# Kernel optimization log

Measured on AMD Instinct MI355X. Metric: run time of the kernel, lower is better.

Reference implementation:

```python
import jax, jax.numpy as jnp
import numpy as np

EMBED = 1024
HEADS = 16
HEAD_DIM = EMBED // HEADS
LN_EPS = 1e-5


def _layer_norm(x, g, b):
    m = jnp.mean(x, axis=-1, keepdims=True)
    v = jnp.mean((x - m) ** 2, axis=-1, keepdims=True)
    return (x - m) / jnp.sqrt(v + LN_EPS) * g + b


def _rope(x):
    # x: (b, H, n, D); standard rotary: freqs repeated (cat(freqs, freqs)), rotate_half
    D = x.shape[-1]
    n = x.shape[2]
    inv_freq = 1.0 / (10000.0 ** (jnp.arange(0, D, 2, dtype=jnp.float32) / D))
    freqs = jnp.arange(n, dtype=jnp.float32)[:, None] * inv_freq[None, :]  # (n, D/2)
    emb = jnp.concatenate([freqs, freqs], axis=-1)  # (n, D)
    cos, sin = jnp.cos(emb), jnp.sin(emb)
    rot = jnp.concatenate([-x[..., D // 2:], x[..., : D // 2]], axis=-1)
    return x * cos + rot * sin


def setup_inputs() -> dict:
    key = jax.random.key(0)
    ks = jax.random.split(key, 8)
    E = EMBED
    s_in = 1.0 / np.sqrt(E)
    return {
        "x": jax.random.normal(ks[0], (2, 2048, E), dtype=jnp.float32),
        "in_proj_w": jax.random.uniform(ks[1], (3 * E, E), jnp.float32, -s_in, s_in),
        "in_proj_b": jnp.zeros((3 * E,), jnp.float32),
        "out_proj_w": jax.random.uniform(ks[2], (E, E), jnp.float32, -s_in, s_in),
        "out_proj_b": jnp.zeros((E,), jnp.float32),
        "geglu_w": jax.random.uniform(ks[3], (2 * E, E), jnp.float32, -s_in, s_in),
        "geglu_b": jnp.zeros((2 * E,), jnp.float32),
        "ln1_g": jnp.ones((E,), jnp.float32),
        "ln1_b": jnp.zeros((E,), jnp.float32),
        "ln2_g": jnp.ones((E,), jnp.float32),
        "ln2_b": jnp.zeros((E,), jnp.float32),
    }


def reference(x, in_proj_w, in_proj_b, out_proj_w, out_proj_b,
              geglu_w, geglu_b, ln1_g, ln1_b, ln2_g, ln2_b):
    b, n, E = x.shape
    H, D = HEADS, HEAD_DIM

    # RoPE applied to raw x (q = k = v = x in the module)
    xh = x.reshape(b, n, H, D).transpose(0, 2, 1, 3)  # (b,H,n,D)
    qr = _rope(xh)
    kr = qr  # q and k are identical pre-projection
    q = qr.transpose(0, 2, 1, 3).reshape(b, n, E)
    k = kr.transpose(0, 2, 1, 3).reshape(b, n, E)
    v = x

    # MultiheadAttention (batch-first semantics): in-proj, per-head SDPA, out-proj
    w_q, w_k, w_v = jnp.split(in_proj_w, 3, axis=0)
    b_q, b_k, b_v = jnp.split(in_proj_b, 3, axis=0)
    qp = (q @ w_q.T + b_q).reshape(b, n, H, D).transpose(0, 2, 1, 3)
    kp = (k @ w_k.T + b_k).reshape(b, n, H, D).transpose(0, 2, 1, 3)
    vp = (v @ w_v.T + b_v).reshape(b, n, H, D).transpose(0, 2, 1, 3)
    scores = jnp.einsum("bhqd,bhkd->bhqk", qp, kp) / jnp.sqrt(jnp.float32(D))
    attn = jax.nn.softmax(scores, axis=-1)
    ctx = jnp.einsum("bhqk,bhkd->bhqd", attn, vp)
    ctx = ctx.transpose(0, 2, 1, 3).reshape(b, n, E)
    attn_out = ctx @ out_proj_w.T + out_proj_b

    # residual + LN1
    h = _layer_norm(x + attn_out, ln1_g, ln1_b)

    # GeGLU: Linear(E -> 2E), chunk, value * gelu(gate) (exact erf gelu like torch)
    proj = h @ geglu_w.T + geglu_b
    val, gate = jnp.split(proj, 2, axis=-1)
    fc_out = val * jax.nn.gelu(gate, approximate=False)

    # residual + LN2
    return _layer_norm(h + fc_out, ln2_g, ln2_b)
```

## Files before the change

kernel.cpp:

```cpp
#include <hip/hip_runtime.h>


typedef __bf16 bf16;
typedef bf16 bf16x8 __attribute__((ext_vector_type(8)));
typedef bf16 bf16x4 __attribute__((ext_vector_type(4)));
typedef float f32x4 __attribute__((ext_vector_type(4)));
typedef float f32x16 __attribute__((ext_vector_type(16)));

#define EMB 1024
#define SEQ 2048
#define NTOK 4096
#define NH 16
#define HD 64

__device__ __forceinline__ f32x4 mfma16(bf16x8 a, bf16x8 b, f32x4 c) {
  return __builtin_amdgcn_mfma_f32_16x16x32_bf16(a, b, c, 0, 0, 0);
}
__device__ __forceinline__ f32x16 mfma32(bf16x8 a, bf16x8 b, f32x16 c) {
  return __builtin_amdgcn_mfma_f32_32x32x16_bf16(a, b, c, 0, 0, 0);
}

__device__ __forceinline__ void gll16(const void* g, void* l) {
  __builtin_amdgcn_global_load_lds(
      (const __attribute__((address_space(1))) void*)g,
      (__attribute__((address_space(3))) void*)l, 16, 0, 0);
}

__device__ __forceinline__ unsigned pk2(float a, float b) {
  union { bf16 h[2]; unsigned u; } t;
  t.h[0] = (bf16)a; t.h[1] = (bf16)b;
  return t.u;
}


__global__ __launch_bounds__(256) void rope_cast(
    const float* __restrict__ x, bf16* __restrict__ xb, bf16* __restrict__ qr) {
  int idx = blockIdx.x * 256 + threadIdx.x;
  int row = idx >> 9;
  int i = idx & 511;
  int h = i >> 5, d2 = i & 31;
  int pos = row & (SEQ - 1);
  int c0 = h * HD + d2;
  size_t base = (size_t)row * EMB;
  float x0 = x[base + c0], x1 = x[base + c0 + 32];
  float invf = exp2f(-(float)d2 * 0.4152410118609203f);
  float ang = (float)pos * invf;
  float sn, cs;
  sincosf(ang, &sn, &cs);
  qr[base + c0] = (bf16)(x0 * cs - x1 * sn);
  qr[base + c0 + 32] = (bf16)(x1 * cs + x0 * sn);
  xb[base + c0] = (bf16)x0;
  xb[base + c0 + 32] = (bf16)x1;
}

__global__ __launch_bounds__(256) void cast_w(
    const float* __restrict__ w, bf16* __restrict__ o, int n) {
  int i = (blockIdx.x * 256 + threadIdx.x) * 4;
  if (i < n) {
    float4 f = *(const float4*)(w + i);
    o[i] = (bf16)f.x; o[i + 1] = (bf16)f.y;
    o[i + 2] = (bf16)f.z; o[i + 3] = (bf16)f.w;
  }
}

__global__ __launch_bounds__(256) void gemm_in(
    const bf16* __restrict__ Aq, const bf16* __restrict__ Ax,
    const bf16* __restrict__ W, const float* __restrict__ bias,
    bf16* __restrict__ qb, bf16* __restrict__ kv) {
  __shared__ bf16 As[128 * 32];
  __shared__ bf16 Bs[128 * 32];
  const int tid = threadIdx.x, lane = tid & 63, wave = tid >> 6;
  const int quad = lane >> 4, l16 = lane & 15;
  const int m0 = blockIdx.y * 128, n0 = blockIdx.x * 128;
  const bf16* A = (n0 < 2048) ? Aq : Ax;
  const int K = 1024;
  const int wm = (wave >> 1) * 64, wn = (wave & 1) * 64;
  const int srow = wave * 32 + (lane >> 2);
  const int scol = (lane & 3) * 8;
  f32x4 acc[4][4] = {};
  for (int k0 = 0; k0 < K; k0 += 32) {
    __syncthreads();
    gll16(A + (size_t)(m0 + srow) * K + k0 + scol, As + wave * 1024);
    gll16(A + (size_t)(m0 + srow + 16) * K + k0 + scol, As + wave * 1024 + 512);
    gll16(W + (size_t)(n0 + srow) * K + k0 + scol, Bs + wave * 1024);
    gll16(W + (size_t)(n0 + srow + 16) * K + k0 + scol, Bs + wave * 1024 + 512);
    __syncthreads();
    bf16x8 af[4], bw[4];
#pragma unroll
    for (int t = 0; t < 4; ++t) {
      af[t] = *(const bf16x8*)(As + (wm + t * 16 + l16) * 32 + quad * 8);
      bw[t] = *(const bf16x8*)(Bs + (wn + t * 16 + l16) * 32 + quad * 8);
    }
#pragma unroll
    for (int mt = 0; mt < 4; ++mt)
#pragma unroll
      for (int nt = 0; nt < 4; ++nt)
        acc[mt][nt] = mfma16(af[mt], bw[nt], acc[mt][nt]);
  }
  if (n0 < 1024) {
#pragma unroll
    for (int mt = 0; mt < 4; ++mt)
      for (int nt = 0; nt < 4; ++nt) {
        const int n = n0 + wn + nt * 16 + l16;
        const float bv = bias[n];
#pragma unroll
        for (int r = 0; r < 4; ++r) {
          const int m = m0 + wm + mt * 16 + quad * 4 + r;
          qb[(size_t)m * 1024 + n] = (bf16)((acc[mt][nt][r] + bv) * 0.125f);
        }
      }
  } else if (n0 < 2048) {
#pragma unroll
    for (int mt = 0; mt < 4; ++mt)
      for (int nt = 0; nt < 4; ++nt) {
        const int n = n0 + wn + nt * 16 + l16;
        const float bv = bias[n];
        const int kd = n - 1024, hh = kd >> 6, d = kd & 63;
        const int dc = d >> 3, dl = d & 7;
#pragma unroll
        for (int r = 0; r < 4; ++r) {
          const int m = m0 + wm + mt * 16 + quad * 4 + r;
          const int bb = m >> 11, s = m & 2047;
          const int t = s >> 7, kr = s & 127;
          const size_t base = ((size_t)((bb * 16 + hh) * 16 + t)) * 16384;
          kv[base + kr * 64 + ((dc ^ (kr & 7)) << 3) + dl] =
              (bf16)((acc[mt][nt][r] + bv) * 1.4426950408889634f);
        }
      }
  } else {
#pragma unroll
    for (int mt = 0; mt < 4; ++mt)
      for (int nt = 0; nt < 4; ++nt) {
        const int n = n0 + wn + nt * 16 + l16;
        const float bv = bias[n];
        const int vd = n - 2048, hh = vd >> 6, d = vd & 63;
        const int m = m0 + wm + mt * 16 + quad * 4;
        const int bb = m >> 11, s = m & 2047;
        const int t = s >> 7, kt = s & 127;
        const int g = kt >> 4, w = kt & 15;
        const int c = 2 * g + ((w >> 2) & 1);
        const int slot = (w & 8) ? 4 : 0;
        const size_t base = ((size_t)((bb * 16 + hh) * 16 + t)) * 16384 + 8192;
        bf16x4 pkv;
#pragma unroll
        for (int r = 0; r < 4; ++r) pkv[r] = (bf16)(acc[mt][nt][r] + bv);
        *(bf16x4*)(kv + base + d * 128 + ((c ^ (d & 7)) << 3) + slot) = pkv;
      }
  }
}

__global__ __launch_bounds__(256) void gemm_bt(
    const bf16* __restrict__ A, const bf16* __restrict__ W,
    const float* __restrict__ bias,
    float* __restrict__ outF, bf16* __restrict__ outB,
    int M, int N, int K) {
  __shared__ bf16 As[128 * 32];
  __shared__ bf16 Bs[128 * 32];
  const int tid = threadIdx.x, lane = tid & 63, wave = tid >> 6;
  const int quad = lane >> 4, l16 = lane & 15;
  const int m0 = blockIdx.y * 128, n0 = blockIdx.x * 128;
  const int wm = (wave >> 1) * 64, wn = (wave & 1) * 64;
  const int srow = wave * 32 + (lane >> 2);
  const int scol = (lane & 3) * 8;
  f32x4 acc[4][4] = {};
  for (int k0 = 0; k0 < K; k0 += 32) {
    __syncthreads();
    gll16(A + (size_t)(m0 + srow) * K + k0 + scol, As + wave * 1024);
    gll16(A + (size_t)(m0 + srow + 16) * K + k0 + scol, As + wave * 1024 + 512);
    gll16(W + (size_t)(n0 + srow) * K + k0 + scol, Bs + wave * 1024);
    gll16(W + (size_t)(n0 + srow + 16) * K + k0 + scol, Bs + wave * 1024 + 512);
    __syncthreads();
    bf16x8 af[4], bw[4];
#pragma unroll
    for (int t = 0; t < 4; ++t) {
      af[t] = *(const bf16x8*)(As + (wm + t * 16 + l16) * 32 + quad * 8);
      bw[t] = *(const bf16x8*)(Bs + (wn + t * 16 + l16) * 32 + quad * 8);
    }
#pragma unroll
    for (int mt = 0; mt < 4; ++mt)
#pragma unroll
      for (int nt = 0; nt < 4; ++nt)
        acc[mt][nt] = mfma16(af[mt], bw[nt], acc[mt][nt]);
  }
#pragma unroll
  for (int mt = 0; mt < 4; ++mt)
    for (int nt = 0; nt < 4; ++nt) {
      const int n = n0 + wn + nt * 16 + l16;
      const float bv = bias ? bias[n] : 0.0f;
#pragma unroll
      for (int r = 0; r < 4; ++r) {
        const int m = m0 + wm + mt * 16 + quad * 4 + r;
        const float v = acc[mt][nt][r] + bv;
        if (outF) outF[(size_t)m * N + n] = v;
        if (outB) outB[(size_t)m * N + n] = (bf16)v;
      }
    }
}

__global__ __launch_bounds__(256) void gemm_bt64(
    const bf16* __restrict__ A, const bf16* __restrict__ W,
    const float* __restrict__ bias, float* __restrict__ outF,
    int M, int N, int K) {
  __shared__ bf16 As[128 * 32];
  __shared__ bf16 Bs[64 * 32];
  const int tid = threadIdx.x, lane = tid & 63, wave = tid >> 6;
  const int quad = lane >> 4, l16 = lane & 15;
  const int m0 = blockIdx.y * 128, n0 = blockIdx.x * 64;
  const int wm = (wave >> 1) * 64, wn = (wave & 1) * 32;
  const int srow = wave * 32 + (lane >> 2);
  const int srowB = wave * 16 + (lane >> 2);
  const int scol = (lane & 3) * 8;
  f32x4 acc[4][2] = {};
  for (int k0 = 0; k0 < K; k0 += 32) {
    __syncthreads();
    gll16(A + (size_t)(m0 + srow) * K + k0 + scol, As + wave * 1024);
    gll16(A + (size_t)(m0 + srow + 16) * K + k0 + scol, As + wave * 1024 + 512);
    gll16(W + (size_t)(n0 + srowB) * K + k0 + scol, Bs + wave * 512);
    __syncthreads();
    bf16x8 af[4], bw[2];
#pragma unroll
    for (int t = 0; t < 4; ++t)
      af[t] = *(const bf16x8*)(As + (wm + t * 16 + l16) * 32 + quad * 8);
#pragma unroll
    for (int t = 0; t < 2; ++t)
      bw[t] = *(const bf16x8*)(Bs + (wn + t * 16 + l16) * 32 + quad * 8);
#pragma unroll
    for (int mt = 0; mt < 4; ++mt)
#pragma unroll
      for (int nt = 0; nt < 2; ++nt)
        acc[mt][nt] = mfma16(af[mt], bw[nt], acc[mt][nt]);
  }
#pragma unroll
  for (int mt = 0; mt < 4; ++mt)
    for (int nt = 0; nt < 2; ++nt) {
      const int n = n0 + wn + nt * 16 + l16;
      const float bv = bias[n];
#pragma unroll
      for (int r = 0; r < 4; ++r) {
        const int m = m0 + wm + mt * 16 + quad * 4 + r;
        outF[(size_t)m * N + n] = acc[mt][nt][r] + bv;
      }
    }
}

__global__ __launch_bounds__(256) void attn10(
    const bf16* __restrict__ Q, const bf16* __restrict__ KV,
    bf16* __restrict__ ctx) {
  __shared__ __align__(16) bf16 kvb[2][16384];
  const int tid = threadIdx.x, lane = tid & 63, wave = tid >> 6;
  const int hi = lane >> 5, l31 = lane & 31, l7 = lane & 7;
  const int bid = blockIdx.x;
  const int hb = (bid & 7) * 4 + ((bid >> 3) & 3);
  const int qt = bid >> 5;
  const int h = hb & 15, b = hb >> 4;

  bf16x8 qf[4];
  {
    const int qrow = qt * 128 + wave * 32 + l31;
    const bf16* qp = Q + (size_t)(b * SEQ + qrow) * 1024 + h * HD + hi * 8;
#pragma unroll
    for (int t = 0; t < 4; ++t) qf[t] = *(const bf16x8*)(qp + t * 16);
  }
  const bf16* kvg = KV + ((size_t)(b * NH + h) * 16) * 16384 + wave * 2048 + lane * 8;
#pragma unroll
  for (int i = 0; i < 4; ++i) {
    gll16(kvg + i * 512, kvb[0] + wave * 2048 + i * 512);
    gll16(kvg + 8192 + i * 512, kvb[0] + 8192 + wave * 2048 + i * 512);
  }
  f32x16 o0 = {}, o1 = {}, lacc = {};
  const f32x16 zf = {};
  const bf16 onec = (bf16)1.0f;
  const bf16x8 onef = {onec, onec, onec, onec, onec, onec, onec, onec};

  for (int t = 0; t < 16; ++t) {
    __syncthreads();
    if (t + 1 < 16) {
      const bf16* src = kvg + (size_t)(t + 1) * 16384;
      bf16* dst = kvb[(t + 1) & 1] + wave * 2048;
#pragma unroll
      for (int i = 0; i < 4; ++i) {
        gll16(src + i * 512, dst + i * 512);
        gll16(src + 8192 + i * 512, dst + 8192 + i * 512);
      }
    }
    const bf16* ks = kvb[t & 1];
    const bf16* vs = kvb[t & 1] + 8192;
#pragma unroll
    for (int half = 0; half < 2; ++half) {
      const bf16* ksh = ks + half * 4096;
      f32x16 s0, s1;
      {
        const int swc = (hi ^ l7) * 8;
        bf16x8 k0 = *(const bf16x8*)(ksh + l31 * 64 + swc);
        bf16x8 k1 = *(const bf16x8*)(ksh + (32 + l31) * 64 + swc);
        s0 = mfma32(k0, qf[0], zf);
        s1 = mfma32(k1, qf[0], zf);
      }
#pragma unroll
      for (int tt = 1; tt < 4; ++tt) {
        const int swc = ((tt * 2 + hi) ^ l7) * 8;
        bf16x8 k0 = *(const bf16x8*)(ksh + l31 * 64 + swc);
        bf16x8 k1 = *(const bf16x8*)(ksh + (32 + l31) * 64 + swc);
        s0 = mfma32(k0, qf[tt], s0);
        s1 = mfma32(k1, qf[tt], s1);
      }
      unsigned u[16];
#pragma unroll
      for (int g = 0; g < 8; ++g) {
        const int base = (g & 3) * 4;
        float e0, e1, e2, e3;
        if (g < 4) {
          e0 = __builtin_amdgcn_exp2f(s0[base]);
          e1 = __builtin_amdgcn_exp2f(s0[base + 1]);
          e2 = __builtin_amdgcn_exp2f(s0[base + 2]);
          e3 = __builtin_amdgcn_exp2f(s0[base + 3]);
        } else {
          e0 = __builtin_amdgcn_exp2f(s1[base]);
          e1 = __builtin_amdgcn_exp2f(s1[base + 1]);
          e2 = __builtin_amdgcn_exp2f(s1[base + 2]);
          e3 = __builtin_amdgcn_exp2f(s1[base + 3]);
        }
        u[g * 2] = pk2(e0, e1);
        u[g * 2 + 1] = pk2(e2, e3);
      }
#pragma unroll
      for (int kk = 0; kk < 4; ++kk) {
        union { unsigned w[4]; bf16x8 v; } fw;
        fw.w[0] = u[4 * kk]; fw.w[1] = u[4 * kk + 1];
        fw.w[2] = u[4 * kk + 2]; fw.w[3] = u[4 * kk + 3];
        const int c16 = (8 * half + 2 * kk + hi) ^ l7;
        bf16x8 v0 = *(const bf16x8*)(vs + l31 * 128 + c16 * 8);
        bf16x8 v1 = *(const bf16x8*)(vs + (32 + l31) * 128 + c16 * 8);
        lacc = mfma32(fw.v, onef, lacc);
        o0 = mfma32(fw.v, v0, o0);
        o1 = mfma32(fw.v, v1, o1);
      }
    }
  }
#pragma unroll
  for (int r = 0; r < 16; ++r) {
    const int qloc = (r & 3) + 8 * (r >> 2) + 4 * hi;
    const float inv = 1.0f / lacc[r];
    const int qrow = qt * 128 + wave * 32 + qloc;
    bf16* cp = ctx + (size_t)(b * SEQ + qrow) * EMB + h * HD;
    cp[l31] = (bf16)(o0[r] * inv);
    cp[32 + l31] = (bf16)(o1[r] * inv);
  }
}

__global__ __launch_bounds__(256) void ln1_k(
    const float* __restrict__ x, const float* __restrict__ ao,
    const float* __restrict__ g, const float* __restrict__ bta,
    float* __restrict__ hF, bf16* __restrict__ hB) {
  int row = blockIdx.x, tid = threadIdx.x;
  const float* xr = x + (size_t)row * EMB;
  const float* ar = ao + (size_t)row * EMB;
  float v[4], s = 0.0f, s2 = 0.0f;
#pragma unroll
  for (int i = 0; i < 4; ++i) {
    float t = xr[tid + i * 256] + ar[tid + i * 256];
    v[i] = t; s += t; s2 += t * t;
  }
#pragma unroll
  for (int off = 1; off < 64; off <<= 1) {
    s += __shfl_xor(s, off, 64);
    s2 += __shfl_xor(s2, off, 64);
  }
  __shared__ float red[8];
  int wave = tid >> 6, lane = tid & 63;
  if (lane == 0) { red[wave] = s; red[4 + wave] = s2; }
  __syncthreads();
  s = red[0] + red[1] + red[2] + red[3];
  s2 = red[4] + red[5] + red[6] + red[7];
  float mean = s * (1.0f / EMB);
  float var = s2 * (1.0f / EMB) - mean * mean;
  float inv = rsqrtf(var + 1e-5f);
#pragma unroll
  for (int i = 0; i < 4; ++i) {
    int c = tid + i * 256;
    float t = (v[i] - mean) * inv * g[c] + bta[c];
    hF[(size_t)row * EMB + c] = t;
    hB[(size_t)row * EMB + c] = (bf16)t;
  }
}

__global__ __launch_bounds__(256) void geglu_ln2(
    const float* __restrict__ h, const bf16* __restrict__ proj,
    const float* __restrict__ g, const float* __restrict__ bta,
    float* __restrict__ out) {
  int row = blockIdx.x, tid = threadIdx.x;
  const float* hr = h + (size_t)row * EMB;
  const bf16* pr = proj + (size_t)row * 2048;
  float v[4], s = 0.0f, s2 = 0.0f;
#pragma unroll
  for (int i = 0; i < 4; ++i) {
    int c = tid + i * 256;
    float val = (float)pr[c];
    float gate = (float)pr[1024 + c];
    float ge = 0.5f * gate * (1.0f + erff(gate * 0.70710678f));
    float t = hr[c] + val * ge;
    v[i] = t; s += t; s2 += t * t;
  }
#pragma unroll
  for (int off = 1; off < 64; off <<= 1) {
    s += __shfl_xor(s, off, 64);
    s2 += __shfl_xor(s2, off, 64);
  }
  __shared__ float red[8];
  int wave = tid >> 6, lane = tid & 63;
  if (lane == 0) { red[wave] = s; red[4 + wave] = s2; }
  __syncthreads();
  s = red[0] + red[1] + red[2] + red[3];
  s2 = red[4] + red[5] + red[6] + red[7];
  float mean = s * (1.0f / EMB);
  float var = s2 * (1.0f / EMB) - mean * mean;
  float inv = rsqrtf(var + 1e-5f);
#pragma unroll
  for (int i = 0; i < 4; ++i) {
    int c = tid + i * 256;
    out[(size_t)row * EMB + c] = (v[i] - mean) * inv * g[c] + bta[c];
  }
}

extern "C" void kernel_launch(void* const* d_in, const int* in_sizes, int n_in,
                              void* d_out, int out_size, void* d_ws, size_t ws_size,
                              hipStream_t stream) {
  const float* x = (const float*)d_in[0];
  const float* inW = (const float*)d_in[1];
  const float* inB = (const float*)d_in[2];
  const float* outW = (const float*)d_in[3];
  const float* opB = (const float*)d_in[4];
  const float* ggW = (const float*)d_in[5];
  const float* ggB = (const float*)d_in[6];
  const float* g1 = (const float*)d_in[7];
  const float* b1 = (const float*)d_in[8];
  const float* g2 = (const float*)d_in[9];
  const float* b2 = (const float*)d_in[10];
  float* out = (float*)d_out;
  char* ws = (char*)d_ws;
  const size_t MB = 1ull << 20;
  bf16* xb = (bf16*)(ws);
  bf16* hB = (bf16*)(ws);
  bf16* qr = (bf16*)(ws + 8 * MB);
  bf16* ctx = (bf16*)(ws + 8 * MB);
  bf16* wI = (bf16*)(ws + 16 * MB);
  bf16* wO = (bf16*)(ws + 22 * MB);
  bf16* wG = (bf16*)(ws + 24 * MB);
  bf16* qb = (bf16*)(ws + 28 * MB);
  bf16* kv = (bf16*)(ws + 36 * MB);
  bf16* projB = (bf16*)(ws + 28 * MB);
  float* ao = (float*)(ws + 52 * MB);

  rope_cast<<<NTOK * 512 / 256, 256, 0, stream>>>(x, xb, qr);
  cast_w<<<(3072 * 1024 / 4) / 256, 256, 0, stream>>>(inW, wI, 3072 * 1024);
  cast_w<<<(1024 * 1024 / 4) / 256, 256, 0, stream>>>(outW, wO, 1024 * 1024);
  cast_w<<<(2048 * 1024 / 4) / 256, 256, 0, stream>>>(ggW, wG, 2048 * 1024);
  gemm_in<<<dim3(24, 32), 256, 0, stream>>>(qr, xb, wI, inB, qb, kv);
  attn10<<<512, 256, 0, stream>>>(qb, kv, ctx);
  gemm_bt64<<<dim3(16, 32), 256, 0, stream>>>(ctx, wO, opB, ao,
                                              NTOK, 1024, 1024);
  ln1_k<<<NTOK, 256, 0, stream>>>(x, ao, g1, b1, ao, hB);
  gemm_bt<<<dim3(16, 32), 256, 0, stream>>>(hB, wG, ggB, nullptr, projB,
                                            NTOK, 2048, 1024);
  geglu_ln2<<<NTOK, 256, 0, stream>>>(ao, projB, g2, b2, out);
}
```

Before: 278.9 us.

## Split attention KV sequence across two wave groups and fuse weight casts

The attention kernel now runs 512 threads per block: two groups of four waves each process half of the KV sequence in 64-key tiles, and their partial outputs and row sums are combined through shared memory at the end. The K/V staging layout written by the input projection is changed to 64-row tiles to match. s_setprio hints are placed around the MFMA sections, and the three weight-cast launches are merged into one kernel. The aim is more waves in flight to hide latency and fewer launches, at the cost of an extra shared-memory reduction and more synchronisation.

```diff
diff --git a/kernel.cpp b/kernel.cpp
--- a/kernel.cpp
+++ b/kernel.cpp
@@ -53,14 +53,18 @@
   xb[base + c0 + 32] = (bf16)x1;
 }
 
-__global__ __launch_bounds__(256) void cast_w(
-    const float* __restrict__ w, bf16* __restrict__ o, int n) {
+__global__ __launch_bounds__(256) void cast_all(
+    const float* __restrict__ w0, const float* __restrict__ w1,
+    const float* __restrict__ w2, bf16* __restrict__ o0,
+    bf16* __restrict__ o1, bf16* __restrict__ o2) {
   int i = (blockIdx.x * 256 + threadIdx.x) * 4;
-  if (i < n) {
-    float4 f = *(const float4*)(w + i);
-    o[i] = (bf16)f.x; o[i + 1] = (bf16)f.y;
-    o[i + 2] = (bf16)f.z; o[i + 3] = (bf16)f.w;
-  }
+  const float* s; bf16* d; int off;
+  if (i < 3 * 1024 * 1024) { s = w0; d = o0; off = i; }
+  else if (i < 4 * 1024 * 1024) { s = w1; d = o1; off = i - 3 * 1024 * 1024; }
+  else { s = w2; d = o2; off = i - 4 * 1024 * 1024; }
+  float4 f = *(const float4*)(s + off);
+  d[off] = (bf16)f.x; d[off + 1] = (bf16)f.y;
+  d[off + 2] = (bf16)f.z; d[off + 3] = (bf16)f.w;
 }
 
 __global__ __launch_bounds__(256) void gemm_in(
@@ -121,8 +125,8 @@
         for (int r = 0; r < 4; ++r) {
           const int m = m0 + wm + mt * 16 + quad * 4 + r;
           const int bb = m >> 11, s = m & 2047;
-          const int t = s >> 7, kr = s & 127;
-          const size_t base = ((size_t)((bb * 16 + hh) * 16 + t)) * 16384;
+          const int t = s >> 6, kr = s & 63;
+          const size_t base = ((size_t)((bb * 16 + hh) * 32 + t)) * 8192;
           kv[base + kr * 64 + ((dc ^ (kr & 7)) << 3) + dl] =
               (bf16)((acc[mt][nt][r] + bv) * 1.4426950408889634f);
         }
@@ -136,15 +140,15 @@
         const int vd = n - 2048, hh = vd >> 6, d = vd & 63;
         const int m = m0 + wm + mt * 16 + quad * 4;
         const int bb = m >> 11, s = m & 2047;
-        const int t = s >> 7, kt = s & 127;
+        const int t = s >> 6, kt = s & 63;
         const int g = kt >> 4, w = kt & 15;
         const int c = 2 * g + ((w >> 2) & 1);
         const int slot = (w & 8) ? 4 : 0;
-        const size_t base = ((size_t)((bb * 16 + hh) * 16 + t)) * 16384 + 8192;
+        const size_t base = ((size_t)((bb * 16 + hh) * 32 + t)) * 8192 + 4096;
         bf16x4 pkv;
 #pragma unroll
         for (int r = 0; r < 4; ++r) pkv[r] = (bf16)(acc[mt][nt][r] + bv);
-        *(bf16x4*)(kv + base + d * 128 + ((c ^ (d & 7)) << 3) + slot) = pkv;
+        *(bf16x4*)(kv + base + d * 64 + ((c ^ (d & 7)) << 3) + slot) = pkv;
       }
   }
 }
@@ -243,11 +247,12 @@
     }
 }
 
-__global__ __launch_bounds__(256) void attn10(
+__global__ __launch_bounds__(512, 4) void attn11(
     const bf16* __restrict__ Q, const bf16* __restrict__ KV,
     bf16* __restrict__ ctx) {
-  __shared__ __align__(16) bf16 kvb[2][16384];
+  __shared__ __align__(16) bf16 kvb[2][2][8192];
   const int tid = threadIdx.x, lane = tid & 63, wave = tid >> 6;
+  const int grp = wave >> 2, lw = wave & 3;
   const int hi = lane >> 5, l31 = lane & 31, l7 = lane & 7;
   const int bid = blockIdx.x;
   const int hb = (bid & 7) * 4 + ((bid >> 3) & 3);
@@ -256,17 +261,18 @@
 
   bf16x8 qf[4];
   {
-    const int qrow = qt * 128 + wave * 32 + l31;
+    const int qrow = qt * 128 + lw * 32 + l31;
     const bf16* qp = Q + (size_t)(b * SEQ + qrow) * 1024 + h * HD + hi * 8;
 #pragma unroll
     for (int t = 0; t < 4; ++t) qf[t] = *(const bf16x8*)(qp + t * 16);
   }
-  const bf16* kvg = KV + ((size_t)(b * NH + h) * 16) * 16384 + wave * 2048 + lane * 8;
-#pragma unroll
-  for (int i = 0; i < 4; ++i) {
-    gll16(kvg + i * 512, kvb[0] + wave * 2048 + i * 512);
-    gll16(kvg + 8192 + i * 512, kvb[0] + 8192 + wave * 2048 + i * 512);
-  }
+  const int soff = lw * 2048 + lane * 8;
+  const bf16* kvg = KV + ((size_t)((b * NH + h) * 32 + grp * 16)) * 8192 + soff;
+  bf16* myb[2] = {&kvb[grp][0][0], &kvb[grp][1][0]};
+#pragma unroll
+  for (int i = 0; i < 4; ++i)
+    gll16(kvg + i * 512, myb[0] + soff + i * 512);
+
   f32x16 o0 = {}, o1 = {}, lacc = {};
   const f32x16 zf = {};
   const bf16 onec = (bf16)1.0f;
@@ -275,76 +281,86 @@
   for (int t = 0; t < 16; ++t) {
     __syncthreads();
     if (t + 1 < 16) {
-      const bf16* src = kvg + (size_t)(t + 1) * 16384;
-      bf16* dst = kvb[(t + 1) & 1] + wave * 2048;
-#pragma unroll
-      for (int i = 0; i < 4; ++i) {
-        gll16(src + i * 512, dst + i * 512);
-        gll16(src + 8192 + i * 512, dst + 8192 + i * 512);
-      }
-    }
-    const bf16* ks = kvb[t & 1];
-    const bf16* vs = kvb[t & 1] + 8192;
-#pragma unroll
-    for (int half = 0; half < 2; ++half) {
-      const bf16* ksh = ks + half * 4096;
-      f32x16 s0, s1;
-      {
-        const int swc = (hi ^ l7) * 8;
-        bf16x8 k0 = *(const bf16x8*)(ksh + l31 * 64 + swc);
-        bf16x8 k1 = *(const bf16x8*)(ksh + (32 + l31) * 64 + swc);
-        s0 = mfma32(k0, qf[0], zf);
-        s1 = mfma32(k1, qf[0], zf);
-      }
-#pragma unroll
-      for (int tt = 1; tt < 4; ++tt) {
-        const int swc = ((tt * 2 + hi) ^ l7) * 8;
-        bf16x8 k0 = *(const bf16x8*)(ksh + l31 * 64 + swc);
-        bf16x8 k1 = *(const bf16x8*)(ksh + (32 + l31) * 64 + swc);
-        s0 = mfma32(k0, qf[tt], s0);
-        s1 = mfma32(k1, qf[tt], s1);
-      }
-      unsigned u[16];
-#pragma unroll
-      for (int g = 0; g < 8; ++g) {
-        const int base = (g & 3) * 4;
-        float e0, e1, e2, e3;
-        if (g < 4) {
-          e0 = __builtin_amdgcn_exp2f(s0[base]);
-          e1 = __builtin_amdgcn_exp2f(s0[base + 1]);
-          e2 = __builtin_amdgcn_exp2f(s0[base + 2]);
-          e3 = __builtin_amdgcn_exp2f(s0[base + 3]);
-        } else {
-          e0 = __builtin_amdgcn_exp2f(s1[base]);
-          e1 = __builtin_amdgcn_exp2f(s1[base + 1]);
-          e2 = __builtin_amdgcn_exp2f(s1[base + 2]);
-          e3 = __builtin_amdgcn_exp2f(s1[base + 3]);
-        }
-        u[g * 2] = pk2(e0, e1);
-        u[g * 2 + 1] = pk2(e2, e3);
-      }
-#pragma unroll
-      for (int kk = 0; kk < 4; ++kk) {
-        union { unsigned w[4]; bf16x8 v; } fw;
-        fw.w[0] = u[4 * kk]; fw.w[1] = u[4 * kk + 1];
-        fw.w[2] = u[4 * kk + 2]; fw.w[3] = u[4 * kk + 3];
-        const int c16 = (8 * half + 2 * kk + hi) ^ l7;
-        bf16x8 v0 = *(const bf16x8*)(vs + l31 * 128 + c16 * 8);
-        bf16x8 v1 = *(const bf16x8*)(vs + (32 + l31) * 128 + c16 * 8);
-        lacc = mfma32(fw.v, onef, lacc);
-        o0 = mfma32(fw.v, v0, o0);
-        o1 = mfma32(fw.v, v1, o1);
-      }
-    }
-  }
-#pragma unroll
-  for (int r = 0; r < 16; ++r) {
-    const int qloc = (r & 3) + 8 * (r >> 2) + 4 * hi;
-    const float inv = 1.0f / lacc[r];
-    const int qrow = qt * 128 + wave * 32 + qloc;
-    bf16* cp = ctx + (size_t)(b * SEQ + qrow) * EMB + h * HD;
-    cp[l31] = (bf16)(o0[r] * inv);
-    cp[32 + l31] = (bf16)(o1[r] * inv);
+      const bf16* src = kvg + (size_t)(t + 1) * 8192;
+      bf16* dst = myb[(t + 1) & 1] + soff;
+#pragma unroll
+      for (int i = 0; i < 4; ++i) gll16(src + i * 512, dst + i * 512);
+    }
+    const bf16* ks = myb[t & 1];
+    const bf16* vs = ks + 4096;
+    f32x16 s0, s1;
+    __builtin_amdgcn_s_setprio(1);
+    {
+      const int swc = (hi ^ l7) * 8;
+      bf16x8 k0 = *(const bf16x8*)(ks + l31 * 64 + swc);
+      bf16x8 k1 = *(const bf16x8*)(ks + (32 + l31) * 64 + swc);
+      s0 = mfma32(k0, qf[0], zf);
+      s1 = mfma32(k1, qf[0], zf);
+    }
+#pragma unroll
+    for (int tt = 1; tt < 4; ++tt) {
+      const int swc = ((tt * 2 + hi) ^ l7) * 8;
+      bf16x8 k0 = *(const bf16x8*)(ks + l31 * 64 + swc);
+      bf16x8 k1 = *(const bf16x8*)(ks + (32 + l31) * 64 + swc);
+      s0 = mfma32(k0, qf[tt], s0);
+      s1 = mfma32(k1, qf[tt], s1);
+    }
+    __builtin_amdgcn_s_setprio(0);
+    unsigned u[16];
+#pragma unroll
+    for (int g = 0; g < 8; ++g) {
+      const int base = (g & 3) * 4;
+      float e0, e1, e2, e3;
+      if (g < 4) {
+        e0 = __builtin_amdgcn_exp2f(s0[base]);
+        e1 = __builtin_amdgcn_exp2f(s0[base + 1]);
+        e2 = __builtin_amdgcn_exp2f(s0[base + 2]);
+        e3 = __builtin_amdgcn_exp2f(s0[base + 3]);
+      } else {
+        e0 = __builtin_amdgcn_exp2f(s1[base]);
+        e1 = __builtin_amdgcn_exp2f(s1[base + 1]);
+        e2 = __builtin_amdgcn_exp2f(s1[base + 2]);
+        e3 = __builtin_amdgcn_exp2f(s1[base + 3]);
+      }
+      u[g * 2] = pk2(e0, e1);
+      u[g * 2 + 1] = pk2(e2, e3);
+    }
+    __builtin_amdgcn_s_setprio(1);
+#pragma unroll
+    for (int kk = 0; kk < 4; ++kk) {
+      union { unsigned w[4]; bf16x8 v; } fw;
+      fw.w[0] = u[4 * kk]; fw.w[1] = u[4 * kk + 1];
+      fw.w[2] = u[4 * kk + 2]; fw.w[3] = u[4 * kk + 3];
+      const int c16 = (2 * kk + hi) ^ l7;
+      bf16x8 v0 = *(const bf16x8*)(vs + l31 * 64 + c16 * 8);
+      bf16x8 v1 = *(const bf16x8*)(vs + (32 + l31) * 64 + c16 * 8);
+      lacc = mfma32(fw.v, onef, lacc);
+      o0 = mfma32(fw.v, v0, o0);
+      o1 = mfma32(fw.v, v1, o1);
+    }
+    __builtin_amdgcn_s_setprio(0);
+  }
+  __syncthreads();
+  float* fred = (float*)&kvb[0][0][0];
+  if (grp == 1) {
+    float* p = fred + (size_t)(lw * 64 + lane) * 49;
+#pragma unroll
+    for (int r = 0; r < 16; ++r) {
+      p[r] = o0[r]; p[16 + r] = o1[r]; p[32 + r] = lacc[r];
+    }
+  }
+  __syncthreads();
+  if (grp == 0) {
+    const float* p = fred + (size_t)(lw * 64 + lane) * 49;
+#pragma unroll
+    for (int r = 0; r < 16; ++r) {
+      const int qloc = (r & 3) + 8 * (r >> 2) + 4 * hi;
+      const float inv = 1.0f / (lacc[r] + p[32 + r]);
+      const int qrow = qt * 128 + lw * 32 + qloc;
+      bf16* cp = ctx + (size_t)(b * SEQ + qrow) * EMB + h * HD;
+      cp[l31] = (bf16)((o0[r] + p[r]) * inv);
+      cp[32 + l31] = (bf16)((o1[r] + p[16 + r]) * inv);
+    }
   }
 }
 
@@ -452,11 +468,9 @@
   float* ao = (float*)(ws + 52 * MB);
 
   rope_cast<<<NTOK * 512 / 256, 256, 0, stream>>>(x, xb, qr);
-  cast_w<<<(3072 * 1024 / 4) / 256, 256, 0, stream>>>(inW, wI, 3072 * 1024);
-  cast_w<<<(1024 * 1024 / 4) / 256, 256, 0, stream>>>(outW, wO, 1024 * 1024);
-  cast_w<<<(2048 * 1024 / 4) / 256, 256, 0, stream>>>(ggW, wG, 2048 * 1024);
+  cast_all<<<6144, 256, 0, stream>>>(inW, outW, ggW, wI, wO, wG);
   gemm_in<<<dim3(24, 32), 256, 0, stream>>>(qr, xb, wI, inB, qb, kv);
-  attn10<<<512, 256, 0, stream>>>(qb, kv, ctx);
+  attn11<<<512, 512, 0, stream>>>(qb, kv, ctx);
   gemm_bt64<<<dim3(16, 32), 256, 0, stream>>>(ctx, wO, opB, ao,
                                               NTOK, 1024, 1024);
   ln1_k<<<NTOK, 256, 0, stream>>>(x, ao, g1, b1, ao, hB);
```

New measurement: 302.1 us. +8.3%, slower.
